# Kernel tuning notes

Measured on AMD Instinct MI355X. Metric: run time of the kernel, lower is better.

The kernel has to match this reference:

```python
import jax, jax.numpy as jnp
import numpy as np

OUT, IN = 4096, 4096
N_CODES, SUBD = 4096, 8
N_SUB = IN // SUBD  # 512
N_SPARSE = 65536


def setup_inputs() -> dict:
    key = jax.random.key(0)
    ks = jax.random.split(key, 8)
    inp = {
        "input": jax.random.normal(ks[0], (4, 2048, IN), dtype=jnp.float32),
        "codebooks": jax.random.normal(ks[1], (N_CODES, SUBD), dtype=jnp.float32),
        "mappings": jax.random.randint(ks[2], (OUT, N_SUB), 0, N_CODES, dtype=jnp.int32),
        # identity permutation of columns (a valid subvector assignment)
        "subvector_assignment": jnp.arange(IN, dtype=jnp.int32),
        "rowise_norms": jax.random.uniform(ks[3], (IN,), dtype=jnp.float32) + 0.5,
        "colwise_norms": jax.random.uniform(ks[4], (OUT,), dtype=jnp.float32) + 0.5,
        # unique, sorted flat indices into the OUT*IN weight (stride keeps them unique)
        "sparse_idx": (jnp.arange(N_SPARSE, dtype=jnp.int32) * (OUT * IN // N_SPARSE)).astype(jnp.int32),
        "sparse_parameters": jax.random.normal(ks[5], (N_SPARSE,), dtype=jnp.float32),
        "bias": jax.random.normal(ks[6], (OUT,), dtype=jnp.float32),
    }
    return inp


def _construct_weight(codebooks, mappings, subvector_assignment,
                      rowise_norms, colwise_norms, sparse_idx, sparse_parameters):
    out_f, n_sub = mappings.shape
    in_f = subvector_assignment.shape[0]
    # gather-dequant: [out, n_sub, d] -> [out, in]
    recon = codebooks[mappings].reshape(out_f, n_sub * codebooks.shape[-1])
    w = jnp.zeros((out_f, in_f), dtype=codebooks.dtype).at[:, subvector_assignment].set(recon)
    # note: source names are swapped; rowise broadcasts over rows (len in_f)
    w = rowise_norms[None, :] * colwise_norms[:, None] * w
    # sparse outlier scatter (torch: weight[mask] = sparse_parameters, row-major order)
    w = w.reshape(-1).at[sparse_idx].set(sparse_parameters).reshape(out_f, in_f)
    return w


def reference(input, codebooks, mappings, subvector_assignment,
              rowise_norms, colwise_norms, sparse_idx, sparse_parameters, bias):
    w = _construct_weight(codebooks, mappings, subvector_assignment,
                          rowise_norms, colwise_norms, sparse_idx, sparse_parameters)
    # F.linear: x @ W^T + b
    return jnp.einsum("bsi,oi->bso", input, w) + bias
```

## Files before the change

### kernel.cpp

```cpp
#include <hip/hip_runtime.h>
#include <hip/hip_bf16.h>

#define OUT_F 4096
#define IN_F  4096
#define N_SUB 512
#define SUBD  8
#define M_DIM 8192
#define N_SPARSE 65536

typedef __bf16 bf16x8 __attribute__((ext_vector_type(8)));
typedef float floatx4 __attribute__((ext_vector_type(4)));

__global__ __launch_bounds__(256) void build_weight(
    const float* __restrict__ cb,
    const int*   __restrict__ map,
    const int*   __restrict__ sa,
    const float* __restrict__ rn,
    const float* __restrict__ cn,
    __hip_bfloat16* __restrict__ W)
{
    int t  = blockIdx.x * blockDim.x + threadIdx.x;
    int o  = t >> 9;
    int j8 = t & (N_SUB - 1);
    int j  = j8 * SUBD;
    int code = map[o * N_SUB + j8];
    float cno = cn[o];
    float4 c0 = *(const float4*)(cb + code * SUBD);
    float4 c1 = *(const float4*)(cb + code * SUBD + 4);
    int4 s0 = *(const int4*)(sa + j);
    int4 s1 = *(const int4*)(sa + j + 4);
    bool contig = (s0.x == j)     & (s0.y == j + 1) & (s0.z == j + 2) &
                  (s0.w == j + 3) & (s1.x == j + 4) & (s1.y == j + 5) &
                  (s1.z == j + 6) & (s1.w == j + 7);
    if (contig) {
        float4 r0 = *(const float4*)(rn + j);
        float4 r1 = *(const float4*)(rn + j + 4);
        union { __hip_bfloat16 h[8]; uint4 u; } pk;
        pk.h[0] = __float2bfloat16(c0.x * r0.x * cno);
        pk.h[1] = __float2bfloat16(c0.y * r0.y * cno);
        pk.h[2] = __float2bfloat16(c0.z * r0.z * cno);
        pk.h[3] = __float2bfloat16(c0.w * r0.w * cno);
        pk.h[4] = __float2bfloat16(c1.x * r1.x * cno);
        pk.h[5] = __float2bfloat16(c1.y * r1.y * cno);
        pk.h[6] = __float2bfloat16(c1.z * r1.z * cno);
        pk.h[7] = __float2bfloat16(c1.w * r1.w * cno);
        *(uint4*)(W + (long)o * IN_F + j) = pk.u;
    } else {
        float c[8] = {c0.x, c0.y, c0.z, c0.w, c1.x, c1.y, c1.z, c1.w};
        int   s[8] = {s0.x, s0.y, s0.z, s0.w, s1.x, s1.y, s1.z, s1.w};
#pragma unroll
        for (int e = 0; e < SUBD; e++)
            W[(long)o * IN_F + s[e]] = __float2bfloat16(c[e] * rn[s[e]] * cno);
    }
}

__global__ __launch_bounds__(256) void sparse_scatter(
    const int*   __restrict__ idx,
    const float* __restrict__ sp,
    __hip_bfloat16* __restrict__ W, int n)
{
    int t = blockIdx.x * blockDim.x + threadIdx.x;
    if (t < n) W[idx[t]] = __float2bfloat16(sp[t]);
}

__global__ __launch_bounds__(256) void cvt_bf16(
    const float* __restrict__ in, __hip_bfloat16* __restrict__ out, long n)
{
    long i = ((long)blockIdx.x * blockDim.x + threadIdx.x) * 8;
    if (i >= n) return;
    float4 f0 = *(const float4*)(in + i);
    float4 f1 = *(const float4*)(in + i + 4);
    union { __hip_bfloat16 h[8]; uint4 u; } pk;
    pk.h[0] = __float2bfloat16(f0.x); pk.h[1] = __float2bfloat16(f0.y);
    pk.h[2] = __float2bfloat16(f0.z); pk.h[3] = __float2bfloat16(f0.w);
    pk.h[4] = __float2bfloat16(f1.x); pk.h[5] = __float2bfloat16(f1.y);
    pk.h[6] = __float2bfloat16(f1.z); pk.h[7] = __float2bfloat16(f1.w);
    *(uint4*)(out + i) = pk.u;
}

__device__ __forceinline__ void gl2lds16(const __hip_bfloat16* g, __hip_bfloat16* l)
{
    __builtin_amdgcn_global_load_lds(
        (const __attribute__((address_space(1))) unsigned int*)g,
        (__attribute__((address_space(3))) unsigned int*)l,
        16, 0, 0);
}

__global__ __launch_bounds__(256, 4) void gemm_bt_bias(
    const __hip_bfloat16* __restrict__ A,
    const __hip_bfloat16* __restrict__ B,
    const float* __restrict__ bias,
    float* __restrict__ C)
{
    constexpr int N = OUT_F, K = IN_F;
    constexpr int BK = 64;

    __shared__ __hip_bfloat16 sA[128 * BK];
    __shared__ __hip_bfloat16 sB[128 * BK];

    const int tid  = threadIdx.x;
    const int bm   = blockIdx.y;
    const int bn   = blockIdx.x;
    const int wave = tid >> 6;
    const int lane = tid & 63;
    const int wm   = (wave >> 1) * 64;
    const int wn   = (wave & 1) * 64;
    const int l16  = lane & 15;
    const int quad = lane >> 4;

    floatx4 acc[4][4] = {};

    const int sr = tid >> 3;
    const int sc = (((tid & 7) ^ ((tid >> 3) & 7))) * 8;
    const __hip_bfloat16* gA = A + (long)(bm * 128 + sr) * K + sc;
    const __hip_bfloat16* gB = B + (long)(bn * 128 + sr) * K + sc;
    __hip_bfloat16* lA = sA + tid * 8;
    __hip_bfloat16* lB = sB + tid * 8;

    for (int kt = 0; kt < K; kt += BK) {
#pragma unroll
        for (int i = 0; i < 4; i++)
            gl2lds16(gA + kt + (long)i * 32 * K, lA + i * 2048);
#pragma unroll
        for (int i = 0; i < 4; i++)
            gl2lds16(gB + kt + (long)i * 32 * K, lB + i * 2048);
        __syncthreads();

#pragma unroll
        for (int ks = 0; ks < 2; ks++) {
            bf16x8 af[4], bfr[4];
#pragma unroll
            for (int mt = 0; mt < 4; mt++) {
                int r = wm + mt * 16 + l16;
                af[mt] = *(const bf16x8*)(sA + r * BK + (((ks * 4 + quad) ^ (l16 & 7)) * 8));
            }
#pragma unroll
            for (int nt = 0; nt < 4; nt++) {
                int r = wn + nt * 16 + l16;
                bfr[nt] = *(const bf16x8*)(sB + r * BK + (((ks * 4 + quad) ^ (l16 & 7)) * 8));
            }
#pragma unroll
            for (int mt = 0; mt < 4; mt++)
#pragma unroll
                for (int nt = 0; nt < 4; nt++)
                    acc[mt][nt] = __builtin_amdgcn_mfma_f32_16x16x32_bf16(
                        af[mt], bfr[nt], acc[mt][nt], 0, 0, 0);
        }

        __syncthreads();
    }

#pragma unroll
    for (int mt = 0; mt < 4; mt++) {
#pragma unroll
        for (int nt = 0; nt < 4; nt++) {
            int row = bm * 128 + wm + mt * 16 + quad * 4;
            int col = bn * 128 + wn + nt * 16 + l16;
            float bv = bias[col];
            float* cp = C + (long)row * N + col;
#pragma unroll
            for (int r = 0; r < 4; r++)
                cp[(long)r * N] = acc[mt][nt][r] + bv;
        }
    }
}

extern "C" void kernel_launch(void* const* d_in, const int* in_sizes, int n_in,
                              void* d_out, int out_size, void* d_ws, size_t ws_size,
                              hipStream_t stream)
{
    const float* input = (const float*)d_in[0];
    const float* cb    = (const float*)d_in[1];
    const int*   map   = (const int*)  d_in[2];
    const int*   sa    = (const int*)  d_in[3];
    const float* rn    = (const float*)d_in[4];
    const float* cn    = (const float*)d_in[5];
    const int*   sidx  = (const int*)  d_in[6];
    const float* sp    = (const float*)d_in[7];
    const float* bias  = (const float*)d_in[8];
    float* out = (float*)d_out;

    __hip_bfloat16* W  = (__hip_bfloat16*)d_ws;
    __hip_bfloat16* Ab = (__hip_bfloat16*)((char*)d_ws + (size_t)OUT_F * IN_F * 2);

    build_weight<<<(OUT_F * N_SUB) / 256, 256, 0, stream>>>(cb, map, sa, rn, cn, W);
    sparse_scatter<<<N_SPARSE / 256, 256, 0, stream>>>(sidx, sp, W, N_SPARSE);
    const long n_act = (long)M_DIM * IN_F;
    cvt_bf16<<<(int)(n_act / 8 / 256), 256, 0, stream>>>(input, Ab, n_act);
    dim3 grid(OUT_F / 128, M_DIM / 128);
    gemm_bt_bias<<<grid, 256, 0, stream>>>(Ab, W, bias, out);
}
```

Baseline: 487.1 us.

## Replace GEMM with 256x256 tiled, double-buffered, phase-interleaved MFMA pipeline

Swaps the 128x128 single-buffered GEMM for a 256x256 tile kernel using 512 threads and double-buffered LDS. Each K step is split into four phases that interleave half-tile global-to-LDS loads with MFMA quadrants, using barriers, s_setprio and vmcnt waits. A block-index swizzle groups neighbouring tiles for L2 reuse. This aims to hide load latency and raise arithmetic intensity, at the cost of higher register pressure and LDS use (128KB per block). It also relies on a hand-tuned barrier ordering.

```diff
diff --git a/kernel.cpp b/kernel.cpp
--- a/kernel.cpp
+++ b/kernel.cpp
@@ -78,6 +78,11 @@
     *(uint4*)(out + i) = pk.u;
 }
 
+#define BM 256
+#define BN 256
+#define BK 64
+#define NT (IN_F / BK)
+
 __device__ __forceinline__ void gl2lds16(const __hip_bfloat16* g, __hip_bfloat16* l)
 {
     __builtin_amdgcn_global_load_lds(
@@ -86,81 +91,170 @@
         16, 0, 0);
 }
 
-__global__ __launch_bounds__(256, 4) void gemm_bt_bias(
+__device__ __forceinline__ void stage_half_A(
+    const __hip_bfloat16* __restrict__ Ab, int row0, int kk,
+    __hip_bfloat16* lds, int h, int u, int p)
+{
+#pragma unroll
+    for (int j = 0; j < 2; j++) {
+        const int gr = j * 128 + h * 64 + u;
+        gl2lds16(Ab + (size_t)(row0 + gr) * IN_F + kk + ((p ^ (gr & 7)) << 3),
+                 lds + gr * BK + p * 8);
+    }
+}
+
+__device__ __forceinline__ void stage_half_B(
+    const __hip_bfloat16* __restrict__ Bb, int row0, int kk,
+    __hip_bfloat16* lds, int h, int u, int p)
+{
+#pragma unroll
+    for (int j = 0; j < 2; j++) {
+        const int rl = j * 64 + u;
+        const int gr = (rl & 31) + h * 32 + ((rl >> 5) << 6);
+        gl2lds16(Bb + (size_t)(row0 + gr) * IN_F + kk + ((p ^ (gr & 7)) << 3),
+                 lds + gr * BK + p * 8);
+    }
+}
+
+__device__ __forceinline__ void load_af(bf16x8 (&dst)[4][2],
+    const __hip_bfloat16* sbuf, int rowbase, const int (&koff)[2])
+{
+#pragma unroll
+    for (int i = 0; i < 4; i++) {
+        const __hip_bfloat16* rp = sbuf + (rowbase + i * 16) * BK;
+        dst[i][0] = *(const bf16x8*)(rp + koff[0]);
+        dst[i][1] = *(const bf16x8*)(rp + koff[1]);
+    }
+}
+
+__device__ __forceinline__ void load_bf(bf16x8 (&dst)[2][2],
+    const __hip_bfloat16* sbuf, int rowbase, const int (&koff)[2])
+{
+#pragma unroll
+    for (int n2 = 0; n2 < 2; n2++) {
+        const __hip_bfloat16* rp = sbuf + (rowbase + n2 * 16) * BK;
+        dst[n2][0] = *(const bf16x8*)(rp + koff[0]);
+        dst[n2][1] = *(const bf16x8*)(rp + koff[1]);
+    }
+}
+
+template<int MQ, int NQ>
+__device__ __forceinline__ void mfma_quad(floatx4 (&acc)[8][4],
+    const bf16x8 (&af)[4][2], const bf16x8 (&bfr)[2][2])
+{
+#pragma unroll
+    for (int i = 0; i < 4; i++)
+#pragma unroll
+        for (int n2 = 0; n2 < 2; n2++)
+#pragma unroll
+            for (int ks = 0; ks < 2; ks++)
+                acc[MQ * 4 + i][NQ * 2 + n2] =
+                    __builtin_amdgcn_mfma_f32_16x16x32_bf16(
+                        af[i][ks], bfr[n2][ks], acc[MQ * 4 + i][NQ * 2 + n2],
+                        0, 0, 0);
+}
+
+__global__ __launch_bounds__(512, 2) void gemm256_8ph(
     const __hip_bfloat16* __restrict__ A,
     const __hip_bfloat16* __restrict__ B,
     const float* __restrict__ bias,
     float* __restrict__ C)
 {
-    constexpr int N = OUT_F, K = IN_F;
-    constexpr int BK = 64;
-
-    __shared__ __hip_bfloat16 sA[128 * BK];
-    __shared__ __hip_bfloat16 sB[128 * BK];
+    __shared__ __hip_bfloat16 sm[2][2][BM * BK];
 
     const int tid  = threadIdx.x;
-    const int bm   = blockIdx.y;
-    const int bn   = blockIdx.x;
     const int wave = tid >> 6;
     const int lane = tid & 63;
-    const int wm   = (wave >> 1) * 64;
-    const int wn   = (wave & 1) * 64;
     const int l16  = lane & 15;
     const int quad = lane >> 4;
-
-    floatx4 acc[4][4] = {};
-
-    const int sr = tid >> 3;
-    const int sc = (((tid & 7) ^ ((tid >> 3) & 7))) * 8;
-    const __hip_bfloat16* gA = A + (long)(bm * 128 + sr) * K + sc;
-    const __hip_bfloat16* gB = B + (long)(bn * 128 + sr) * K + sc;
-    __hip_bfloat16* lA = sA + tid * 8;
-    __hip_bfloat16* lB = sB + tid * 8;
-
-    for (int kt = 0; kt < K; kt += BK) {
-#pragma unroll
-        for (int i = 0; i < 4; i++)
-            gl2lds16(gA + kt + (long)i * 32 * K, lA + i * 2048);
-#pragma unroll
-        for (int i = 0; i < 4; i++)
-            gl2lds16(gB + kt + (long)i * 32 * K, lB + i * 2048);
-        __syncthreads();
-
-#pragma unroll
-        for (int ks = 0; ks < 2; ks++) {
-            bf16x8 af[4], bfr[4];
-#pragma unroll
-            for (int mt = 0; mt < 4; mt++) {
-                int r = wm + mt * 16 + l16;
-                af[mt] = *(const bf16x8*)(sA + r * BK + (((ks * 4 + quad) ^ (l16 & 7)) * 8));
-            }
-#pragma unroll
-            for (int nt = 0; nt < 4; nt++) {
-                int r = wn + nt * 16 + l16;
-                bfr[nt] = *(const bf16x8*)(sB + r * BK + (((ks * 4 + quad) ^ (l16 & 7)) * 8));
-            }
-#pragma unroll
-            for (int mt = 0; mt < 4; mt++)
-#pragma unroll
-                for (int nt = 0; nt < 4; nt++)
-                    acc[mt][nt] = __builtin_amdgcn_mfma_f32_16x16x32_bf16(
-                        af[mt], bfr[nt], acc[mt][nt], 0, 0, 0);
-        }
-
-        __syncthreads();
-    }
-
-#pragma unroll
-    for (int mt = 0; mt < 4; mt++) {
+    const int u    = wave * 8 + (lane >> 3);
+    const int p    = lane & 7;
+
+    const int wg  = blockIdx.x;
+    const int swz = (wg & 7) * 64 + (wg >> 3);
+    const int bm  = swz >> 4;
+    const int bn  = swz & 15;
+    const int rowA0 = bm * BM;
+    const int rowB0 = bn * BN;
+
+    const int wm = (wave >> 2) * 128;
+    const int wn = (wave & 3) * 64;
+
+    floatx4 acc[8][4] = {};
+    const int koff[2] = { ((0 * 4 + quad) ^ p) * 8, ((1 * 4 + quad) ^ p) * 8 };
+
+    stage_half_A(A, rowA0, 0,  &sm[0][0][0], 0, u, p);
+    stage_half_B(B, rowB0, 0,  &sm[0][1][0], 0, u, p);
+    stage_half_A(A, rowA0, 0,  &sm[0][0][0], 1, u, p);
+    stage_half_B(B, rowB0, 0,  &sm[0][1][0], 1, u, p);
+    stage_half_A(A, rowA0, BK, &sm[1][0][0], 0, u, p);
+    stage_half_B(B, rowB0, BK, &sm[1][1][0], 0, u, p);
+    asm volatile("s_waitcnt vmcnt(4)" ::: "memory");
+    __builtin_amdgcn_s_barrier();
+
+    bf16x8 af0[4][2], af1[4][2], bf0[2][2], bf1[2][2];
+
+    int kt = 0;
+    for (int t = 0; t < NT; ++t) {
+        const int cur = t & 1;
+        __hip_bfloat16* sAc = &sm[cur][0][0];
+        __hip_bfloat16* sBc = &sm[cur][1][0];
+        __hip_bfloat16* sAn = &sm[cur ^ 1][0][0];
+        __hip_bfloat16* sBn = &sm[cur ^ 1][1][0];
+        int k1 = kt + BK;     if (k1 >= IN_F) k1 = 0;
+        int k2 = kt + 2 * BK; if (k2 >= IN_F) k2 = 0;
+
+        load_af(af0, sAc, wm + l16, koff);
+        load_bf(bf0, sBc, wn + l16, koff);
+        stage_half_A(A, rowA0, k1, sAn, 1, u, p);
+        __builtin_amdgcn_s_barrier();
+        asm volatile("s_waitcnt lgkmcnt(0)" ::: "memory");
+        __builtin_amdgcn_s_setprio(1);
+        mfma_quad<0, 0>(acc, af0, bf0);
+        __builtin_amdgcn_s_setprio(0);
+        __builtin_amdgcn_s_barrier();
+
+        load_bf(bf1, sBc, wn + 32 + l16, koff);
+        stage_half_B(B, rowB0, k1, sBn, 1, u, p);
+        __builtin_amdgcn_s_barrier();
+        asm volatile("s_waitcnt lgkmcnt(0)" ::: "memory");
+        __builtin_amdgcn_s_setprio(1);
+        mfma_quad<0, 1>(acc, af0, bf1);
+        __builtin_amdgcn_s_setprio(0);
+        __builtin_amdgcn_s_barrier();
+
+        load_af(af1, sAc, wm + 64 + l16, koff);
+        stage_half_A(A, rowA0, k2, sAc, 0, u, p);
+        __builtin_amdgcn_s_barrier();
+        asm volatile("s_waitcnt lgkmcnt(0)" ::: "memory");
+        __builtin_amdgcn_s_setprio(1);
+        mfma_quad<1, 0>(acc, af1, bf0);
+        __builtin_amdgcn_s_setprio(0);
+        __builtin_amdgcn_s_barrier();
+
+        stage_half_B(B, rowB0, k2, sBc, 0, u, p);
+        __builtin_amdgcn_s_barrier();
+        __builtin_amdgcn_s_setprio(1);
+        mfma_quad<1, 1>(acc, af1, bf1);
+        __builtin_amdgcn_s_setprio(0);
+        asm volatile("s_waitcnt vmcnt(4)" ::: "memory");
+        __builtin_amdgcn_s_barrier();
+
+        kt += BK;
+    }
+    asm volatile("s_waitcnt vmcnt(0)" ::: "memory");
+
+#pragma unroll
+    for (int mt = 0; mt < 8; mt++) {
+        const int row = rowA0 + wm + mt * 16 + quad * 4;
 #pragma unroll
         for (int nt = 0; nt < 4; nt++) {
-            int row = bm * 128 + wm + mt * 16 + quad * 4;
-            int col = bn * 128 + wn + nt * 16 + l16;
-            float bv = bias[col];
-            float* cp = C + (long)row * N + col;
+            const int col = rowB0 + wn + nt * 16 + l16;
+            const float bv = bias[col];
+            float* cp = C + (size_t)row * OUT_F + col;
 #pragma unroll
             for (int r = 0; r < 4; r++)
-                cp[(long)r * N] = acc[mt][nt][r] + bv;
+                cp[(size_t)r * OUT_F] = acc[mt][nt][r] + bv;
         }
     }
 }
@@ -187,6 +281,5 @@
     sparse_scatter<<<N_SPARSE / 256, 256, 0, stream>>>(sidx, sp, W, N_SPARSE);
     const long n_act = (long)M_DIM * IN_F;
     cvt_bf16<<<(int)(n_act / 8 / 256), 256, 0, stream>>>(input, Ab, n_act);
-    dim3 grid(OUT_F / 128, M_DIM / 128);
-    gemm_bt_bias<<<grid, 256, 0, stream>>>(Ab, W, bias, out);
-}
+    gemm256_8ph<<<dim3((M_DIM / BM) * (OUT_F / BN)), 512, 0, stream>>>(Ab, W, bias, out);
+}
```

Result: no change. 485.9 us (-0.2%).
